# Kernel optimization log

Hardware: AMD Instinct MI355X
Metric: run time of the kernel (lower is better)

Reference implementation:

```python
import jax, jax.numpy as jnp
import numpy as np

IN_F, OUT_F, TASK_D, RANK, HID = 1024, 1024, 256, 8, 64
ALPHA = 8.0
SCALING = ALPHA / RANK  # 1.0


def setup_inputs() -> dict:
    key = jax.random.key(0)
    ks = jax.random.split(key, 12)
    s = 0.02
    return {
        "x": jax.random.normal(ks[0], (4, 2048, IN_F), dtype=jnp.float32),
        "base_out": jax.random.normal(ks[1], (4, 2048, OUT_F), dtype=jnp.float32),
        "task_emb": jax.random.normal(ks[2], (4, TASK_D), dtype=jnp.float32),
        # gen_a MLP: Linear(task_dim->hid) + GELU + Linear(hid->out*r)
        "Wa1": jax.random.normal(ks[3], (HID, TASK_D), dtype=jnp.float32) * s,
        "ba1": jnp.zeros((HID,), dtype=jnp.float32),
        "Wa2": jax.random.normal(ks[4], (OUT_F * RANK, HID), dtype=jnp.float32) * s,
        "ba2": jnp.zeros((OUT_F * RANK,), dtype=jnp.float32),
        # gen_b MLP: Linear(task_dim->hid) + GELU + Linear(hid->r*in)
        "Wb1": jax.random.normal(ks[5], (HID, TASK_D), dtype=jnp.float32) * s,
        "bb1": jnp.zeros((HID,), dtype=jnp.float32),
        "Wb2": jax.random.normal(ks[6], (RANK * IN_F, HID), dtype=jnp.float32) * s,
        "bb2": jnp.zeros((RANK * IN_F,), dtype=jnp.float32),
    }


def reference(x, base_out, task_emb, Wa1, ba1, Wa2, ba2, Wb1, bb1, Wb2, bb2):
    lead = x.shape[:-1]
    x2d = x.reshape(-1, IN_F)                      # (b_eff, in)
    b_eff = x2d.shape[0]
    # broadcast task_emb to b_eff rows (repeat + trim, as in torch)
    B = task_emb.shape[0]
    reps = (b_eff + B - 1) // B
    task_eff = jnp.tile(task_emb, (reps, 1))[:b_eff]  # (b_eff, task_dim)

    gelu = lambda t: jax.nn.gelu(t, approximate=False)
    h_a = gelu(task_eff @ Wa1.T + ba1)
    vec_a = h_a @ Wa2.T + ba2                      # (b_eff, out*r)
    h_b = gelu(task_eff @ Wb1.T + bb1)
    vec_b = h_b @ Wb2.T + bb2                      # (b_eff, r*in)

    a = vec_a.reshape(b_eff, OUT_F, RANK)
    b = vec_b.reshape(b_eff, RANK, IN_F)

    # dropout p=0 (eval): x passes through
    tmp = jnp.einsum('bi,bri->br', x2d, b)         # (b_eff, r)
    y_delta = jnp.einsum('br,bor->bo', tmp, a)     # (b_eff, out)
    y = base_out.reshape(-1, OUT_F) + SCALING * y_delta
    return y.reshape(*lead, OUT_F)
```

## Files before the change

kernel.cpp:

```cpp
#include <hip/hip_runtime.h>
#include <math.h>

#define IN_F   1024
#define OUT_F  1024
#define TASK_D 256
#define RANK   8
#define HID    64

__device__ __forceinline__ float gelu_exact(float v) {
    return 0.5f * v * (1.0f + erff(v * 0.70710678118654752f));
}

__global__ __launch_bounds__(256) void gen_kernel(
    const float* __restrict__ task_emb,
    const float* __restrict__ Wa1, const float* __restrict__ ba1,
    const float* __restrict__ Wa2, const float* __restrict__ ba2,
    const float* __restrict__ Wb1, const float* __restrict__ bb1,
    const float* __restrict__ Wb2, const float* __restrict__ bb2,
    float* __restrict__ vec_a_t, float* __restrict__ vec_b)
{
    const int gen = blockIdx.x >> 7;
    const int blk = blockIdx.x & 127;
    const float* __restrict__ W1 = gen ? Wb1 : Wa1;
    const float* __restrict__ b1 = gen ? bb1 : ba1;
    const float* __restrict__ W2 = gen ? Wb2 : Wa2;
    const float* __restrict__ b2 = gen ? bb2 : ba2;

    __shared__ float hs[4][HID];
    {
        const int j = threadIdx.x >> 2;
        const int t = threadIdx.x & 3;
        const float4* te = (const float4*)(task_emb + t * TASK_D);
        const float4* w  = (const float4*)(W1 + j * TASK_D);
        float acc = 0.f;
        #pragma unroll
        for (int d = 0; d < TASK_D / 4; ++d) {
            float4 a = te[d], b = w[d];
            acc += a.x * b.x + a.y * b.y + a.z * b.z + a.w * b.w;
        }
        hs[t][j] = gelu_exact(acc + b1[j]);
    }
    __syncthreads();

    const int lrow = threadIdx.x >> 2;
    const int q    = threadIdx.x & 3;
    const int o    = blk * 64 + lrow;

    const float4* w2 = (const float4*)(W2 + (size_t)o * HID + q * 16);
    float acc0 = 0.f, acc1 = 0.f, acc2 = 0.f, acc3 = 0.f;
    #pragma unroll
    for (int k = 0; k < 4; ++k) {
        float4 w = w2[k];
        const int kb = q * 16 + k * 4;
        acc0 += hs[0][kb] * w.x + hs[0][kb+1] * w.y + hs[0][kb+2] * w.z + hs[0][kb+3] * w.w;
        acc1 += hs[1][kb] * w.x + hs[1][kb+1] * w.y + hs[1][kb+2] * w.z + hs[1][kb+3] * w.w;
        acc2 += hs[2][kb] * w.x + hs[2][kb+1] * w.y + hs[2][kb+2] * w.z + hs[2][kb+3] * w.w;
        acc3 += hs[3][kb] * w.x + hs[3][kb+1] * w.y + hs[3][kb+2] * w.z + hs[3][kb+3] * w.w;
    }
    #pragma unroll
    for (int off = 1; off <= 2; off <<= 1) {
        acc0 += __shfl_xor(acc0, off, 64);
        acc1 += __shfl_xor(acc1, off, 64);
        acc2 += __shfl_xor(acc2, off, 64);
        acc3 += __shfl_xor(acc3, off, 64);
    }
    if (q == 0) {
        const float bb = b2[o];
        float v[4] = { acc0 + bb, acc1 + bb, acc2 + bb, acc3 + bb };
        if (gen == 0) {
            const int oo = o >> 3, r = o & 7;
            #pragma unroll
            for (int t = 0; t < 4; ++t)
                vec_a_t[t * (RANK * OUT_F) + r * OUT_F + oo] = v[t];
        } else {
            #pragma unroll
            for (int t = 0; t < 4; ++t)
                vec_b[t * (RANK * IN_F) + o] = v[t];
        }
    }
}

__global__ __launch_bounds__(256) void apply_kernel(
    const float* __restrict__ x, const float* __restrict__ base_out,
    const float* __restrict__ vec_a_t, const float* __restrict__ vec_b,
    float* __restrict__ out)
{
    const int t    = blockIdx.x & 3;
    const int g    = blockIdx.x >> 2;
    const int wave = threadIdx.x >> 6;
    const int lane = threadIdx.x & 63;

    __shared__ float bs[RANK * IN_F];
    {
        const float4* src = (const float4*)(vec_b + (size_t)t * (RANK * IN_F));
        float4* dst = (float4*)bs;
        #pragma unroll
        for (int i = 0; i < 8; ++i)
            dst[threadIdx.x + 256 * i] = src[threadIdx.x + 256 * i];
    }
    __syncthreads();

    const int jbase = g * 8 + wave * 2;
    float tmp[2][RANK];

    #pragma unroll
    for (int i = 0; i < 2; ++i) {
        const int row = t + 4 * (jbase + i);
        const float* __restrict__ xr = x + (size_t)row * IN_F;
        float4 xv[4];
        #pragma unroll
        for (int c = 0; c < 4; ++c)
            xv[c] = *(const float4*)(xr + c * 256 + lane * 4);

        float acc[RANK];
        #pragma unroll
        for (int r = 0; r < RANK; ++r) acc[r] = 0.f;
        #pragma unroll
        for (int c = 0; c < 4; ++c) {
            const int k = c * 256 + lane * 4;
            #pragma unroll
            for (int r = 0; r < RANK; ++r) {
                const float4 bv = *(const float4*)(bs + r * IN_F + k);
                acc[r] += xv[c].x * bv.x + xv[c].y * bv.y + xv[c].z * bv.z + xv[c].w * bv.w;
            }
        }
        #pragma unroll
        for (int off = 32; off > 0; off >>= 1) {
            #pragma unroll
            for (int r = 0; r < RANK; ++r)
                acc[r] += __shfl_xor(acc[r], off, 64);
        }
        #pragma unroll
        for (int r = 0; r < RANK; ++r) tmp[i][r] = acc[r];
    }

    const float* __restrict__ at = vec_a_t + (size_t)t * (RANK * OUT_F);
    #pragma unroll
    for (int c = 0; c < 4; ++c) {
        const int o = c * 256 + lane * 4;
        float4 af[RANK];
        #pragma unroll
        for (int r = 0; r < RANK; ++r)
            af[r] = *(const float4*)(at + r * OUT_F + o);
        #pragma unroll
        for (int i = 0; i < 2; ++i) {
            const int row = t + 4 * (jbase + i);
            const float4 bo = *(const float4*)(base_out + (size_t)row * OUT_F + o);
            float4 rv;
            rv.x = bo.x; rv.y = bo.y; rv.z = bo.z; rv.w = bo.w;
            #pragma unroll
            for (int r = 0; r < RANK; ++r) {
                rv.x += tmp[i][r] * af[r].x;
                rv.y += tmp[i][r] * af[r].y;
                rv.z += tmp[i][r] * af[r].z;
                rv.w += tmp[i][r] * af[r].w;
            }
            *(float4*)(out + (size_t)row * OUT_F + o) = rv;
        }
    }
}

extern "C" void kernel_launch(void* const* d_in, const int* in_sizes, int n_in,
                              void* d_out, int out_size, void* d_ws, size_t ws_size,
                              hipStream_t stream) {
    const float* x        = (const float*)d_in[0];
    const float* base_out = (const float*)d_in[1];
    const float* task_emb = (const float*)d_in[2];
    const float* Wa1      = (const float*)d_in[3];
    const float* ba1      = (const float*)d_in[4];
    const float* Wa2      = (const float*)d_in[5];
    const float* ba2      = (const float*)d_in[6];
    const float* Wb1      = (const float*)d_in[7];
    const float* bb1      = (const float*)d_in[8];
    const float* Wb2      = (const float*)d_in[9];
    const float* bb2      = (const float*)d_in[10];
    float* out = (float*)d_out;

    float* vec_a_t = (float*)d_ws;
    float* vec_b   = vec_a_t + 4 * RANK * OUT_F;

    const int b_eff = in_sizes[0] / IN_F;

    gen_kernel<<<256, 256, 0, stream>>>(task_emb, Wa1, ba1, Wa2, ba2,
                                        Wb1, bb1, Wb2, bb2, vec_a_t, vec_b);
    apply_kernel<<<b_eff / 8, 256, 0, stream>>>(x, base_out, vec_a_t, vec_b, out);
}
```

Baseline: 140.8 us.

## Drop LDS staging of vec_b and map one row per half-wave in apply kernel

The apply kernel no longer copies the 32KB per-task vec_b slice into shared memory and syncs. Each half-wave now owns one row and reads vec_b and vec_a directly from global memory, relying on cache hits. Block-to-task mapping changes from interleaved to contiguous groups, so consecutive blocks share the same task's vectors. This removes the per-block 32KB LDS fill and barrier and raises occupancy, at the cost of more L1/L2 traffic for the B and A vectors.

```diff
diff --git a/kernel.cpp b/kernel.cpp
--- a/kernel.cpp
+++ b/kernel.cpp
@@ -83,80 +83,60 @@
 __global__ __launch_bounds__(256) void apply_kernel(
     const float* __restrict__ x, const float* __restrict__ base_out,
     const float* __restrict__ vec_a_t, const float* __restrict__ vec_b,
-    float* __restrict__ out)
+    float* __restrict__ out, int g_per_task)
 {
-    const int t    = blockIdx.x & 3;
-    const int g    = blockIdx.x >> 2;
+    const int t    = blockIdx.x / g_per_task;
+    const int g    = blockIdx.x % g_per_task;
     const int wave = threadIdx.x >> 6;
     const int lane = threadIdx.x & 63;
+    const int tr   = lane >> 5;
+    const int ln   = lane & 31;
 
-    __shared__ float bs[RANK * IN_F];
-    {
-        const float4* src = (const float4*)(vec_b + (size_t)t * (RANK * IN_F));
-        float4* dst = (float4*)bs;
-        #pragma unroll
-        for (int i = 0; i < 8; ++i)
-            dst[threadIdx.x + 256 * i] = src[threadIdx.x + 256 * i];
-    }
-    __syncthreads();
+    const int j   = g * 8 + wave * 2 + tr;
+    const int row = t + 4 * j;
 
-    const int jbase = g * 8 + wave * 2;
-    float tmp[2][RANK];
+    const float* __restrict__ xr = x + (size_t)row * IN_F;
+    const float* __restrict__ bt = vec_b + (size_t)t * (RANK * IN_F);
+
+    float acc[RANK];
+    #pragma unroll
+    for (int r = 0; r < RANK; ++r) acc[r] = 0.f;
 
     #pragma unroll
-    for (int i = 0; i < 2; ++i) {
-        const int row = t + 4 * (jbase + i);
-        const float* __restrict__ xr = x + (size_t)row * IN_F;
-        float4 xv[4];
+    for (int c = 0; c < 8; ++c) {
+        const int k = c * 128 + ln * 4;
+        const float4 xv = *(const float4*)(xr + k);
         #pragma unroll
-        for (int c = 0; c < 4; ++c)
-            xv[c] = *(const float4*)(xr + c * 256 + lane * 4);
+        for (int r = 0; r < RANK; ++r) {
+            const float4 bv = *(const float4*)(bt + r * IN_F + k);
+            acc[r] += xv.x * bv.x + xv.y * bv.y + xv.z * bv.z + xv.w * bv.w;
+        }
+    }
 
-        float acc[RANK];
+    #pragma unroll
+    for (int off = 1; off <= 16; off <<= 1) {
         #pragma unroll
-        for (int r = 0; r < RANK; ++r) acc[r] = 0.f;
-        #pragma unroll
-        for (int c = 0; c < 4; ++c) {
-            const int k = c * 256 + lane * 4;
-            #pragma unroll
-            for (int r = 0; r < RANK; ++r) {
-                const float4 bv = *(const float4*)(bs + r * IN_F + k);
-                acc[r] += xv[c].x * bv.x + xv[c].y * bv.y + xv[c].z * bv.z + xv[c].w * bv.w;
-            }
-        }
-        #pragma unroll
-        for (int off = 32; off > 0; off >>= 1) {
-            #pragma unroll
-            for (int r = 0; r < RANK; ++r)
-                acc[r] += __shfl_xor(acc[r], off, 64);
-        }
-        #pragma unroll
-        for (int r = 0; r < RANK; ++r) tmp[i][r] = acc[r];
+        for (int r = 0; r < RANK; ++r)
+            acc[r] += __shfl_xor(acc[r], off, 64);
     }
 
     const float* __restrict__ at = vec_a_t + (size_t)t * (RANK * OUT_F);
+    const float* __restrict__ br = base_out + (size_t)row * OUT_F;
+    float* __restrict__ orow = out + (size_t)row * OUT_F;
+
     #pragma unroll
-    for (int c = 0; c < 4; ++c) {
-        const int o = c * 256 + lane * 4;
-        float4 af[RANK];
+    for (int c = 0; c < 8; ++c) {
+        const int o = c * 128 + ln * 4;
+        float4 rv = *(const float4*)(br + o);
         #pragma unroll
-        for (int r = 0; r < RANK; ++r)
-            af[r] = *(const float4*)(at + r * OUT_F + o);
-        #pragma unroll
-        for (int i = 0; i < 2; ++i) {
-            const int row = t + 4 * (jbase + i);
-            const float4 bo = *(const float4*)(base_out + (size_t)row * OUT_F + o);
-            float4 rv;
-            rv.x = bo.x; rv.y = bo.y; rv.z = bo.z; rv.w = bo.w;
-            #pragma unroll
-            for (int r = 0; r < RANK; ++r) {
-                rv.x += tmp[i][r] * af[r].x;
-                rv.y += tmp[i][r] * af[r].y;
-                rv.z += tmp[i][r] * af[r].z;
-                rv.w += tmp[i][r] * af[r].w;
-            }
-            *(float4*)(out + (size_t)row * OUT_F + o) = rv;
+        for (int r = 0; r < RANK; ++r) {
+            const float4 af = *(const float4*)(at + r * OUT_F + o);
+            rv.x += acc[r] * af.x;
+            rv.y += acc[r] * af.y;
+            rv.z += acc[r] * af.z;
+            rv.w += acc[r] * af.w;
         }
+        *(float4*)(orow + o) = rv;
     }
 }
 
@@ -183,5 +163,8 @@
 
     gen_kernel<<<256, 256, 0, stream>>>(task_emb, Wa1, ba1, Wa2, ba2,
                                         Wb1, bb1, Wb2, bb2, vec_a_t, vec_b);
-    apply_kernel<<<b_eff / 8, 256, 0, stream>>>(x, base_out, vec_a_t, vec_b, out);
+
+    const int nblk = b_eff / 8;
+    apply_kernel<<<nblk, 256, 0, stream>>>(x, base_out, vec_a_t, vec_b, out,
+                                           nblk / 4);
 }
```

Measured after the change: 156.1 us. 1.11x slower.
